# Optimization experiments

Hardware: AMD Instinct MI355X
Metric: run time of the kernel (lower is better)

The kernel has to match this reference:

```python
import jax, jax.numpy as jnp
import numpy as np

EPS = 1e-5  # torch BatchNorm2d default eps


def _bn(x, gamma, beta, mean, var):
    # x: (B, C, H, W); params: (C,). Inference-mode batch norm (running stats).
    inv = gamma / jnp.sqrt(var + EPS)
    return x * inv[:, None, None] + (beta - mean * inv)[:, None, None]


def setup_inputs() -> dict:
    key = jax.random.key(0)
    ks = jax.random.split(key, 8)
    B, QC, QH, QW = 8, 64, 64, 64
    VC, VH, VW = 128, 32, 32
    q = jax.random.normal(ks[0], (B, QC, QH, QW), dtype=jnp.float32)
    v = jax.random.normal(ks[1], (B, VC, VH, VW), dtype=jnp.float32)
    # 1x1 conv weights (out_ch, in_ch), bias=False
    k_w = jax.random.normal(ks[2], (QC, VC), dtype=jnp.float32) * (1.0 / np.sqrt(VC))
    v_w = jax.random.normal(ks[3], (QC, VC), dtype=jnp.float32) * (1.0 / np.sqrt(VC))
    # BatchNorm params (inference mode with running stats)
    q_gamma = jnp.ones((QC,), jnp.float32)
    q_beta = jnp.zeros((QC,), jnp.float32)
    q_mean = jax.random.normal(ks[4], (QC,), dtype=jnp.float32) * 0.1
    q_var = jax.random.uniform(ks[5], (QC,), dtype=jnp.float32, minval=0.5, maxval=1.5)
    k_gamma = jnp.ones((QC,), jnp.float32)
    k_beta = jnp.zeros((QC,), jnp.float32)
    k_mean = jax.random.normal(ks[6], (QC,), dtype=jnp.float32) * 0.1
    k_var = jax.random.uniform(ks[7], (QC,), dtype=jnp.float32, minval=0.5, maxval=1.5)
    return {
        "q": q, "v": v, "k_w": k_w, "v_w": v_w,
        "q_gamma": q_gamma, "q_beta": q_beta, "q_mean": q_mean, "q_var": q_var,
        "k_gamma": k_gamma, "k_beta": k_beta, "k_mean": k_mean, "k_var": k_var,
    }


def reference(q, v, k_w, v_w, q_gamma, q_beta, q_mean, q_var,
              k_gamma, k_beta, k_mean, k_var):
    B, C, H, W = q.shape
    Nq = H * W
    # query: BN(q) -> (B, Nq, C)
    qn = _bn(q, q_gamma, q_beta, q_mean, q_var)
    query = qn.reshape(B, C, Nq).transpose(0, 2, 1)
    # key: 1x1 conv + BN -> (B, C, Nv)
    key = jnp.einsum('oc,bchw->bohw', k_w, v)
    key = _bn(key, k_gamma, k_beta, k_mean, k_var)
    Nv = key.shape[2] * key.shape[3]
    key = key.reshape(B, C, Nv)
    # value: 1x1 conv -> (B, Nv, C)
    value = jnp.einsum('oc,bchw->bohw', v_w, v).reshape(B, C, Nv).transpose(0, 2, 1)
    # full spatial attention (NO 1/sqrt(d) scaling, matching source)
    sim = jnp.einsum('bnc,bcm->bnm', query, key)          # (B, Nq, Nv)
    attn = jax.nn.softmax(sim, axis=-1)
    out = jnp.einsum('bnm,bmc->bnc', attn, value)         # (B, Nq, C)
    return out.transpose(0, 2, 1).reshape(B, C, H, W)
```

## Files before the change

### kernel.cpp

```cpp
#include <hip/hip_runtime.h>
#include <hip/hip_bf16.h>

#define EPS 1e-5f

typedef _Float16 f16x8 __attribute__((ext_vector_type(8)));
typedef short short8v __attribute__((ext_vector_type(8)));
typedef float f32x4 __attribute__((ext_vector_type(4)));

static __device__ __forceinline__ unsigned short f2h(float x) {
    _Float16 h = (_Float16)x;
    return *reinterpret_cast<unsigned short*>(&h);
}

__global__ __launch_bounds__(256) void conv_kv_kernel(const float* __restrict__ v,
                               const float* __restrict__ k_w, const float* __restrict__ v_w,
                               const float* __restrict__ kg, const float* __restrict__ kbe,
                               const float* __restrict__ km, const float* __restrict__ kvv,
                               unsigned short* __restrict__ Kt, unsigned short* __restrict__ Vt) {
    __shared__ unsigned short vtile[32 * 136];
    const int t = threadIdx.x;
    const int w = t >> 6, lane = t & 63, g = lane >> 4, qr = lane & 15;
    const int b = blockIdx.y, m0 = blockIdx.x * 32;

    float4 vstg[4];
#pragma unroll
    for (int r = 0; r < 4; ++r) {
        int idx = r * 256 + t;
        int c = idx >> 3, mq = idx & 7;
        vstg[r] = *reinterpret_cast<const float4*>(&v[((size_t)b * 128 + c) * 1024 + m0 + mq * 4]);
    }
    float4 kwl[4][2], vwl[4][2];
#pragma unroll
    for (int ck = 0; ck < 4; ++ck) {
        const float* kp = &k_w[(16 * w + qr) * 128 + 32 * ck + 8 * g];
        const float* vp = &v_w[(16 * w + qr) * 128 + 32 * ck + 8 * g];
        kwl[ck][0] = *reinterpret_cast<const float4*>(kp);
        kwl[ck][1] = *reinterpret_cast<const float4*>(kp + 4);
        vwl[ck][0] = *reinterpret_cast<const float4*>(vp);
        vwl[ck][1] = *reinterpret_cast<const float4*>(vp + 4);
    }
#pragma unroll
    for (int r = 0; r < 4; ++r) {
        int idx = r * 256 + t;
        int c = idx >> 3, mq = idx & 7;
        vtile[(mq * 4 + 0) * 136 + c] = f2h(vstg[r].x);
        vtile[(mq * 4 + 1) * 136 + c] = f2h(vstg[r].y);
        vtile[(mq * 4 + 2) * 136 + c] = f2h(vstg[r].z);
        vtile[(mq * 4 + 3) * 136 + c] = f2h(vstg[r].w);
    }
    __syncthreads();

    f16x8 kwf[4], vwf[4];
#pragma unroll
    for (int ck = 0; ck < 4; ++ck)
#pragma unroll
        for (int j = 0; j < 8; ++j) {
            kwf[ck][j] = (_Float16)(j < 4 ? kwl[ck][0][j] : kwl[ck][1][j - 4]);
            vwf[ck][j] = (_Float16)(j < 4 ? vwl[ck][0][j] : vwl[ck][1][j - 4]);
        }

    f32x4 accK[2], accV[2];
#pragma unroll
    for (int mb = 0; mb < 2; ++mb) {
        f16x8 bf[4];
#pragma unroll
        for (int ck = 0; ck < 4; ++ck)
            bf[ck] = *reinterpret_cast<const f16x8*>(&vtile[(mb * 16 + qr) * 136 + 32 * ck + 8 * g]);
        f32x4 aK = {0.f, 0.f, 0.f, 0.f}, aV = {0.f, 0.f, 0.f, 0.f};
#pragma unroll
        for (int ck = 0; ck < 4; ++ck) {
            aK = __builtin_amdgcn_mfma_f32_16x16x32_f16(kwf[ck], bf[ck], aK, 0, 0, 0);
            aV = __builtin_amdgcn_mfma_f32_16x16x32_f16(vwf[ck], bf[ck], aV, 0, 0, 0);
        }
        accK[mb] = aK; accV[mb] = aV;
    }

    float invk_i[4], biask_i[4];
#pragma unroll
    for (int i = 0; i < 4; ++i) {
        int o = 16 * w + 4 * g + i;
        invk_i[i] = kg[o] * rsqrtf(kvv[o] + EPS);
        biask_i[i] = kbe[o] - km[o] * invk_i[i];
    }
#pragma unroll
    for (int mb = 0; mb < 2; ++mb) {
        int m = m0 + mb * 16 + qr;
#pragma unroll
        for (int i = 0; i < 4; ++i) {
            int o = 16 * w + 4 * g + i;
            Kt[((size_t)b * 1024 + m) * 64 + o] = f2h(accK[mb][i] * invk_i[i] + biask_i[i]);
            Vt[((size_t)b * 64 + o) * 1024 + m] = f2h(accV[mb][i]);
        }
    }
}

__global__ __launch_bounds__(256, 2) void attn_kernel(const float* __restrict__ q,
        const float* __restrict__ qg, const float* __restrict__ qbt,
        const float* __restrict__ qm, const float* __restrict__ qv,
        const unsigned short* __restrict__ Kt, const unsigned short* __restrict__ Vt,
        float* __restrict__ out) {
    __shared__ __align__(16) unsigned char smem[61952];
    unsigned short* S16 = (unsigned short*)smem;
    float* SF = (float*)smem;
    const int t = threadIdx.x;
    const int w = t >> 6, lane = t & 63, g = lane >> 4, qr = lane & 15;
    const int b = blockIdx.y, n0 = blockIdx.x * 64;

    unsigned short* kT = S16 + w * 4864;
    unsigned short* vT = kT + 2304;
    float* ib  = SF + 14848;
    float* mlb = SF + 14976;

    const int koff0 = w * 256;
    const int kr_row = lane >> 3, kr_sub = lane & 7;
    const int vr_row = lane >> 2, vr_sub = lane & 3;

    short8v kpf[4], vpf[4];
#pragma unroll
    for (int ch = 0; ch < 4; ++ch) {
        kpf[ch] = *reinterpret_cast<const short8v*>(
            Kt + (size_t)(b * 1024 + koff0 + ch * 8 + kr_row) * 64 + kr_sub * 8);
        vpf[ch] = *reinterpret_cast<const short8v*>(
            Vt + (size_t)(b * 64 + ch * 16 + vr_row) * 1024 + koff0 + vr_sub * 8);
    }

    if (t < 64) {
        float inv = qg[t] * rsqrtf(qv[t] + EPS);
        ib[t] = inv * 1.44269504f;
        ib[64 + t] = (qbt[t] - qm[t] * inv) * 1.44269504f;
    }
    __syncthreads();

    f16x8 qf0[4], qf1[4];
#pragma unroll
    for (int j = 0; j < 4; ++j) {
        int nq = n0 + j * 16 + qr;
#pragma unroll
        for (int e = 0; e < 8; ++e) {
            int c0 = g * 8 + e, c1 = 32 + g * 8 + e;
            qf0[j][e] = (_Float16)(q[(size_t)(b * 64 + c0) * 4096 + nq] * ib[c0] + ib[64 + c0]);
            qf1[j][e] = (_Float16)(q[(size_t)(b * 64 + c1) * 4096 + nq] * ib[c1] + ib[64 + c1]);
        }
    }

#pragma unroll
    for (int ch = 0; ch < 4; ++ch) {
        *reinterpret_cast<short8v*>(kT + (ch * 8 + kr_row) * 72 + kr_sub * 8) = kpf[ch];
        *reinterpret_cast<short8v*>(vT + (ch * 16 + vr_row) * 40 + vr_sub * 8) = vpf[ch];
    }

    f32x4 oacc[4][4];
#pragma unroll
    for (int j = 0; j < 4; ++j)
#pragma unroll
        for (int cb = 0; cb < 4; ++cb) oacc[j][cb] = (f32x4){0, 0, 0, 0};
    float mr[4] = {-1e30f, -1e30f, -1e30f, -1e30f};
    float lp[4] = {0.f, 0.f, 0.f, 0.f};

    auto body = [&](int j, unsigned short* pTj) {
        f32x4 s0, s1;
        {
            f16x8 kf0 = *reinterpret_cast<const f16x8*>(kT + qr * 72 + g * 8);
            f16x8 kf1 = *reinterpret_cast<const f16x8*>(kT + qr * 72 + 32 + g * 8);
            f32x4 a = {0, 0, 0, 0};
            a  = __builtin_amdgcn_mfma_f32_16x16x32_f16(kf0, qf0[j], a, 0, 0, 0);
            s0 = __builtin_amdgcn_mfma_f32_16x16x32_f16(kf1, qf1[j], a, 0, 0, 0);
        }
        {
            f16x8 kf0 = *reinterpret_cast<const f16x8*>(kT + (16 + qr) * 72 + g * 8);
            f16x8 kf1 = *reinterpret_cast<const f16x8*>(kT + (16 + qr) * 72 + 32 + g * 8);
            f32x4 a = {0, 0, 0, 0};
            a  = __builtin_amdgcn_mfma_f32_16x16x32_f16(kf0, qf0[j], a, 0, 0, 0);
            s1 = __builtin_amdgcn_mfma_f32_16x16x32_f16(kf1, qf1[j], a, 0, 0, 0);
        }
        float lmax = fmaxf(fmaxf(fmaxf(s0[0], s0[1]), fmaxf(s0[2], s0[3])),
                           fmaxf(fmaxf(s1[0], s1[1]), fmaxf(s1[2], s1[3])));
        if (!__all(lmax - mr[j] <= 11.0f)) {
            float tm = fmaxf(lmax, __shfl_xor(lmax, 16));
            tm = fmaxf(tm, __shfl_xor(tm, 32));
            float mn = fmaxf(mr[j], tm);
            float sc = exp2f(mr[j] - mn);
            lp[j] *= sc;
            oacc[j][0] *= sc; oacc[j][1] *= sc; oacc[j][2] *= sc; oacc[j][3] *= sc;
            mr[j] = mn;
        }
        float p0 = exp2f(s0[0] - mr[j]), p1 = exp2f(s0[1] - mr[j]);
        float p2 = exp2f(s0[2] - mr[j]), p3 = exp2f(s0[3] - mr[j]);
        float p4 = exp2f(s1[0] - mr[j]), p5 = exp2f(s1[1] - mr[j]);
        float p6 = exp2f(s1[2] - mr[j]), p7 = exp2f(s1[3] - mr[j]);
        lp[j] += ((p0 + p1) + (p2 + p3)) + ((p4 + p5) + (p6 + p7));
        uint2 w0, w1;
        w0.x = __builtin_bit_cast(unsigned int, __builtin_amdgcn_cvt_pkrtz(p0, p1));
        w0.y = __builtin_bit_cast(unsigned int, __builtin_amdgcn_cvt_pkrtz(p2, p3));
        w1.x = __builtin_bit_cast(unsigned int, __builtin_amdgcn_cvt_pkrtz(p4, p5));
        w1.y = __builtin_bit_cast(unsigned int, __builtin_amdgcn_cvt_pkrtz(p6, p7));
        *reinterpret_cast<uint2*>(pTj + qr * 40 + g * 4) = w0;
        *reinterpret_cast<uint2*>(pTj + qr * 40 + 16 + g * 4) = w1;
        f16x8 pf = *reinterpret_cast<const f16x8*>(pTj + qr * 40 + g * 8);
#pragma unroll
        for (int cb = 0; cb < 4; ++cb) {
            f16x8 vf = *reinterpret_cast<const f16x8*>(vT + (cb * 16 + qr) * 40 + g * 8);
            oacc[j][cb] = __builtin_amdgcn_mfma_f32_16x16x32_f16(vf, pf, oacc[j][cb], 0, 0, 0);
        }
    };

    unsigned short* pTbase = S16 + 19456 + w * 2560;

#pragma unroll 1
    for (int i = 0; i < 8; ++i) {
        if (i < 7) {
            int ko = koff0 + (i + 1) * 32;
#pragma unroll
            for (int ch = 0; ch < 4; ++ch) {
                kpf[ch] = *reinterpret_cast<const short8v*>(
                    Kt + (size_t)(b * 1024 + ko + ch * 8 + kr_row) * 64 + kr_sub * 8);
                vpf[ch] = *reinterpret_cast<const short8v*>(
                    Vt + (size_t)(b * 64 + ch * 16 + vr_row) * 1024 + ko + vr_sub * 8);
            }
        }
        body(0, pTbase);
        body(1, pTbase + 640);
        body(2, pTbase + 1280);
        body(3, pTbase + 1920);
        if (i < 7) {
#pragma unroll
            for (int ch = 0; ch < 4; ++ch) {
                *reinterpret_cast<short8v*>(kT + (ch * 8 + kr_row) * 72 + kr_sub * 8) = kpf[ch];
                *reinterpret_cast<short8v*>(vT + (ch * 16 + vr_row) * 40 + vr_sub * 8) = vpf[ch];
            }
        }
    }

    float lred[4];
#pragma unroll
    for (int j = 0; j < 4; ++j) {
        float l = lp[j] + __shfl_xor(lp[j], 16);
        lred[j] = l + __shfl_xor(l, 32);
    }
    __syncthreads();
    if (g == 0) {
#pragma unroll
        for (int j = 0; j < 4; ++j) {
            mlb[((w * 4 + j) * 16 + qr) * 2] = mr[j];
            mlb[((w * 4 + j) * 16 + qr) * 2 + 1] = lred[j];
        }
    }
    __syncthreads();
    float scale_j[4];
#pragma unroll
    for (int j = 0; j < 4; ++j) {
        float m0 = mlb[((0 * 4 + j) * 16 + qr) * 2], l0 = mlb[((0 * 4 + j) * 16 + qr) * 2 + 1];
        float m1 = mlb[((1 * 4 + j) * 16 + qr) * 2], l1 = mlb[((1 * 4 + j) * 16 + qr) * 2 + 1];
        float m2 = mlb[((2 * 4 + j) * 16 + qr) * 2], l2 = mlb[((2 * 4 + j) * 16 + qr) * 2 + 1];
        float m3 = mlb[((3 * 4 + j) * 16 + qr) * 2], l3 = mlb[((3 * 4 + j) * 16 + qr) * 2 + 1];
        float M = fmaxf(fmaxf(m0, m1), fmaxf(m2, m3));
        float e0 = exp2f(m0 - M), e1 = exp2f(m1 - M), e2 = exp2f(m2 - M), e3 = exp2f(m3 - M);
        float L = e0 * l0 + e1 * l1 + e2 * l2 + e3 * l3;
        float ew = (w == 0) ? e0 : (w == 1) ? e1 : (w == 2) ? e2 : e3;
        scale_j[j] = ew / L;
#pragma unroll
        for (int cb = 0; cb < 4; ++cb) oacc[j][cb] *= scale_j[j];
    }
    float* ob = SF;
#pragma unroll 1
    for (int r = 0; r < 4; ++r) {
        if (w == r) {
#pragma unroll
            for (int j = 0; j < 4; ++j)
#pragma unroll
                for (int cb = 0; cb < 4; ++cb) {
                    float* dst = &ob[(j * 16 + qr) * 68 + cb * 16 + g * 4];
                    if (r == 0) *reinterpret_cast<f32x4*>(dst) = oacc[j][cb];
                    else {
                        f32x4 cur = *reinterpret_cast<const f32x4*>(dst);
                        *reinterpret_cast<f32x4*>(dst) = cur + oacc[j][cb];
                    }
                }
        }
        __syncthreads();
    }
    const int row = lane;
#pragma unroll
    for (int k = 0; k < 4; ++k) {
        f32x4 val = *reinterpret_cast<const f32x4*>(&ob[row * 68 + w * 16 + k * 4]);
#pragma unroll
        for (int e = 0; e < 4; ++e) {
            int c = w * 16 + k * 4 + e;
            out[(size_t)(b * 64 + c) * 4096 + n0 + row] = val[e];
        }
    }
}

extern "C" void kernel_launch(void* const* d_in, const int* in_sizes, int n_in,
                              void* d_out, int out_size, void* d_ws, size_t ws_size,
                              hipStream_t stream) {
    const float* q   = (const float*)d_in[0];
    const float* v   = (const float*)d_in[1];
    const float* k_w = (const float*)d_in[2];
    const float* v_w = (const float*)d_in[3];
    const float* qg  = (const float*)d_in[4];
    const float* qb  = (const float*)d_in[5];
    const float* qm  = (const float*)d_in[6];
    const float* qv  = (const float*)d_in[7];
    const float* kg  = (const float*)d_in[8];
    const float* kbe = (const float*)d_in[9];
    const float* km  = (const float*)d_in[10];
    const float* kvv = (const float*)d_in[11];

    unsigned short* Kt = (unsigned short*)d_ws;
    unsigned short* Vt = Kt + (size_t)8 * 1024 * 64;

    conv_kv_kernel<<<dim3(32, 8), 256, 0, stream>>>(v, k_w, v_w, kg, kbe, km, kvv, Kt, Vt);
    attn_kernel<<<dim3(64, 8), 256, 0, stream>>>(q, qg, qb, qm, qv, Kt, Vt, (float*)d_out);
}
```

Before: 40.27 us.

## Keep softmax probabilities in registers using 16x16x16 MFMA, drop LDS P staging

Stops round-tripping the fp16 probability tile through shared memory. The S-accumulator register layout is fed directly as the B operand of two 16x16x16 MFMAs, with V fragments split to match. K and V fragments are now loaded from LDS once per tile and reused across the four query sub-blocks. This removes the P store/load traffic and shrinks shared memory, which may allow higher occupancy. The cost is twice as many (smaller) MFMA instructions for the PV product and more live registers.

```diff
diff --git a/kernel.cpp b/kernel.cpp
--- a/kernel.cpp
+++ b/kernel.cpp
@@ -4,6 +4,7 @@
 #define EPS 1e-5f
 
 typedef _Float16 f16x8 __attribute__((ext_vector_type(8)));
+typedef _Float16 f16x4 __attribute__((ext_vector_type(4)));
 typedef short short8v __attribute__((ext_vector_type(8)));
 typedef float f32x4 __attribute__((ext_vector_type(4)));
 
@@ -99,7 +100,7 @@
         const float* __restrict__ qm, const float* __restrict__ qv,
         const unsigned short* __restrict__ Kt, const unsigned short* __restrict__ Vt,
         float* __restrict__ out) {
-    __shared__ __align__(16) unsigned char smem[61952];
+    __shared__ __align__(16) unsigned char smem[41472];
     unsigned short* S16 = (unsigned short*)smem;
     float* SF = (float*)smem;
     const int t = threadIdx.x;
@@ -108,8 +109,8 @@
 
     unsigned short* kT = S16 + w * 4864;
     unsigned short* vT = kT + 2304;
-    float* ib  = SF + 14848;
-    float* mlb = SF + 14976;
+    float* ib  = SF + 9728;
+    float* mlb = SF + 9856;
 
     const int koff0 = w * 256;
     const int kr_row = lane >> 3, kr_sub = lane & 7;
@@ -157,57 +158,18 @@
     float mr[4] = {-1e30f, -1e30f, -1e30f, -1e30f};
     float lp[4] = {0.f, 0.f, 0.f, 0.f};
 
-    auto body = [&](int j, unsigned short* pTj) {
-        f32x4 s0, s1;
-        {
-            f16x8 kf0 = *reinterpret_cast<const f16x8*>(kT + qr * 72 + g * 8);
-            f16x8 kf1 = *reinterpret_cast<const f16x8*>(kT + qr * 72 + 32 + g * 8);
-            f32x4 a = {0, 0, 0, 0};
-            a  = __builtin_amdgcn_mfma_f32_16x16x32_f16(kf0, qf0[j], a, 0, 0, 0);
-            s0 = __builtin_amdgcn_mfma_f32_16x16x32_f16(kf1, qf1[j], a, 0, 0, 0);
-        }
-        {
-            f16x8 kf0 = *reinterpret_cast<const f16x8*>(kT + (16 + qr) * 72 + g * 8);
-            f16x8 kf1 = *reinterpret_cast<const f16x8*>(kT + (16 + qr) * 72 + 32 + g * 8);
-            f32x4 a = {0, 0, 0, 0};
-            a  = __builtin_amdgcn_mfma_f32_16x16x32_f16(kf0, qf0[j], a, 0, 0, 0);
-            s1 = __builtin_amdgcn_mfma_f32_16x16x32_f16(kf1, qf1[j], a, 0, 0, 0);
-        }
-        float lmax = fmaxf(fmaxf(fmaxf(s0[0], s0[1]), fmaxf(s0[2], s0[3])),
-                           fmaxf(fmaxf(s1[0], s1[1]), fmaxf(s1[2], s1[3])));
-        if (!__all(lmax - mr[j] <= 11.0f)) {
-            float tm = fmaxf(lmax, __shfl_xor(lmax, 16));
-            tm = fmaxf(tm, __shfl_xor(tm, 32));
-            float mn = fmaxf(mr[j], tm);
-            float sc = exp2f(mr[j] - mn);
-            lp[j] *= sc;
-            oacc[j][0] *= sc; oacc[j][1] *= sc; oacc[j][2] *= sc; oacc[j][3] *= sc;
-            mr[j] = mn;
-        }
-        float p0 = exp2f(s0[0] - mr[j]), p1 = exp2f(s0[1] - mr[j]);
-        float p2 = exp2f(s0[2] - mr[j]), p3 = exp2f(s0[3] - mr[j]);
-        float p4 = exp2f(s1[0] - mr[j]), p5 = exp2f(s1[1] - mr[j]);
-        float p6 = exp2f(s1[2] - mr[j]), p7 = exp2f(s1[3] - mr[j]);
-        lp[j] += ((p0 + p1) + (p2 + p3)) + ((p4 + p5) + (p6 + p7));
-        uint2 w0, w1;
-        w0.x = __builtin_bit_cast(unsigned int, __builtin_amdgcn_cvt_pkrtz(p0, p1));
-        w0.y = __builtin_bit_cast(unsigned int, __builtin_amdgcn_cvt_pkrtz(p2, p3));
-        w1.x = __builtin_bit_cast(unsigned int, __builtin_amdgcn_cvt_pkrtz(p4, p5));
-        w1.y = __builtin_bit_cast(unsigned int, __builtin_amdgcn_cvt_pkrtz(p6, p7));
-        *reinterpret_cast<uint2*>(pTj + qr * 40 + g * 4) = w0;
-        *reinterpret_cast<uint2*>(pTj + qr * 40 + 16 + g * 4) = w1;
-        f16x8 pf = *reinterpret_cast<const f16x8*>(pTj + qr * 40 + g * 8);
-#pragma unroll
-        for (int cb = 0; cb < 4; ++cb) {
-            f16x8 vf = *reinterpret_cast<const f16x8*>(vT + (cb * 16 + qr) * 40 + g * 8);
-            oacc[j][cb] = __builtin_amdgcn_mfma_f32_16x16x32_f16(vf, pf, oacc[j][cb], 0, 0, 0);
-        }
-    };
-
-    unsigned short* pTbase = S16 + 19456 + w * 2560;
-
 #pragma unroll 1
     for (int i = 0; i < 8; ++i) {
+        f16x8 kfA0 = *reinterpret_cast<const f16x8*>(kT + qr * 72 + g * 8);
+        f16x8 kfA1 = *reinterpret_cast<const f16x8*>(kT + qr * 72 + 32 + g * 8);
+        f16x8 kfB0 = *reinterpret_cast<const f16x8*>(kT + (16 + qr) * 72 + g * 8);
+        f16x8 kfB1 = *reinterpret_cast<const f16x8*>(kT + (16 + qr) * 72 + 32 + g * 8);
+        f16x4 vfA[4], vfB[4];
+#pragma unroll
+        for (int cb = 0; cb < 4; ++cb) {
+            vfA[cb] = *reinterpret_cast<const f16x4*>(vT + (cb * 16 + qr) * 40 + g * 4);
+            vfB[cb] = *reinterpret_cast<const f16x4*>(vT + (cb * 16 + qr) * 40 + 16 + g * 4);
+        }
         if (i < 7) {
             int ko = koff0 + (i + 1) * 32;
 #pragma unroll
@@ -218,10 +180,48 @@
                     Vt + (size_t)(b * 64 + ch * 16 + vr_row) * 1024 + ko + vr_sub * 8);
             }
         }
-        body(0, pTbase);
-        body(1, pTbase + 640);
-        body(2, pTbase + 1280);
-        body(3, pTbase + 1920);
+#pragma unroll
+        for (int j = 0; j < 4; ++j) {
+            f32x4 s0, s1;
+            {
+                f32x4 a = {0, 0, 0, 0};
+                a  = __builtin_amdgcn_mfma_f32_16x16x32_f16(kfA0, qf0[j], a, 0, 0, 0);
+                s0 = __builtin_amdgcn_mfma_f32_16x16x32_f16(kfA1, qf1[j], a, 0, 0, 0);
+            }
+            {
+                f32x4 a = {0, 0, 0, 0};
+                a  = __builtin_amdgcn_mfma_f32_16x16x32_f16(kfB0, qf0[j], a, 0, 0, 0);
+                s1 = __builtin_amdgcn_mfma_f32_16x16x32_f16(kfB1, qf1[j], a, 0, 0, 0);
+            }
+            float lmax = fmaxf(fmaxf(fmaxf(s0[0], s0[1]), fmaxf(s0[2], s0[3])),
+                               fmaxf(fmaxf(s1[0], s1[1]), fmaxf(s1[2], s1[3])));
+            if (!__all(lmax - mr[j] <= 11.0f)) {
+                float tm = fmaxf(lmax, __shfl_xor(lmax, 16));
+                tm = fmaxf(tm, __shfl_xor(tm, 32));
+                float mn = fmaxf(mr[j], tm);
+                float sc = exp2f(mr[j] - mn);
+                lp[j] *= sc;
+                oacc[j][0] *= sc; oacc[j][1] *= sc; oacc[j][2] *= sc; oacc[j][3] *= sc;
+                mr[j] = mn;
+            }
+            float p0 = exp2f(s0[0] - mr[j]), p1 = exp2f(s0[1] - mr[j]);
+            float p2 = exp2f(s0[2] - mr[j]), p3 = exp2f(s0[3] - mr[j]);
+            float p4 = exp2f(s1[0] - mr[j]), p5 = exp2f(s1[1] - mr[j]);
+            float p6 = exp2f(s1[2] - mr[j]), p7 = exp2f(s1[3] - mr[j]);
+            lp[j] += ((p0 + p1) + (p2 + p3)) + ((p4 + p5) + (p6 + p7));
+            uint2 u0, u1;
+            u0.x = __builtin_bit_cast(unsigned int, __builtin_amdgcn_cvt_pkrtz(p0, p1));
+            u0.y = __builtin_bit_cast(unsigned int, __builtin_amdgcn_cvt_pkrtz(p2, p3));
+            u1.x = __builtin_bit_cast(unsigned int, __builtin_amdgcn_cvt_pkrtz(p4, p5));
+            u1.y = __builtin_bit_cast(unsigned int, __builtin_amdgcn_cvt_pkrtz(p6, p7));
+            f16x4 pf0 = __builtin_bit_cast(f16x4, u0);
+            f16x4 pf1 = __builtin_bit_cast(f16x4, u1);
+#pragma unroll
+            for (int cb = 0; cb < 4; ++cb) {
+                oacc[j][cb] = __builtin_amdgcn_mfma_f32_16x16x16f16(vfA[cb], pf0, oacc[j][cb], 0, 0, 0);
+                oacc[j][cb] = __builtin_amdgcn_mfma_f32_16x16x16f16(vfB[cb], pf1, oacc[j][cb], 0, 0, 0);
+            }
+        }
         if (i < 7) {
 #pragma unroll
             for (int ch = 0; ch < 4; ++ch) {
@@ -246,7 +246,6 @@
         }
     }
     __syncthreads();
-    float scale_j[4];
 #pragma unroll
     for (int j = 0; j < 4; ++j) {
         float m0 = mlb[((0 * 4 + j) * 16 + qr) * 2], l0 = mlb[((0 * 4 + j) * 16 + qr) * 2 + 1];
@@ -257,9 +256,9 @@
         float e0 = exp2f(m0 - M), e1 = exp2f(m1 - M), e2 = exp2f(m2 - M), e3 = exp2f(m3 - M);
         float L = e0 * l0 + e1 * l1 + e2 * l2 + e3 * l3;
         float ew = (w == 0) ? e0 : (w == 1) ? e1 : (w == 2) ? e2 : e3;
-        scale_j[j] = ew / L;
-#pragma unroll
-        for (int cb = 0; cb < 4; ++cb) oacc[j][cb] *= scale_j[j];
+        float sc = ew / L;
+#pragma unroll
+        for (int cb = 0; cb < 4; ++cb) oacc[j][cb] *= sc;
     }
     float* ob = SF;
 #pragma unroll 1
```

Result: faster. 38.29 us (-4.9%).
